# Performance work log

Measured on AMD Instinct MI355X. Metric: run time of the kernel, lower is better.

The kernel has to match this reference:

```python
import jax, jax.numpy as jnp
import numpy as np

P = np.pi
PARENTS = np.array([0,0,0,0,1,2,3,4,5,6,7,8,9,9,9,12,13,14,16,17,18,19,20,21])
VERTS_LIST = np.array([1325,336,1032,4515,1374,4848,1739,5209,1960,5423])
SYNTH = np.array([3,15,4,5,7,8,18,19,20,21])

def _bounds():
    b = [[-0.5933865286111969,0.5933865286111969],[-2*P,2*P],[-1.215762200416361,1.215762200416361],
         [-1.5793940868065197,0.3097956806],[-0.5881754611,0.5689768556],[-0.5323249722,0.6736965222],
         [-1.5793940868065197,0.3097956806],[-0.5689768556,0.5881754611],[-0.6736965222,0.5323249722],
         [-P/3,P/3],[-P/36,P/36],[-P/36,P/36],
         [-0.02268926111,2.441713561],[-0.01,0.01],[-0.01,0.01],
         [-0.02268926111,2.441713561],[-0.01,0.01],[-0.01,0.01],
         [-P/3,P/3],[-P/36,P/36],[-P/36,P/36]]
    b += [[-P/6,P/6]]*6
    b += [[-P/3,P/3],[-P/36,P/36],[-P/36,P/36]]
    b += [[-0.01,0.01]]*6
    b += [[-P/3,P/3],[-P/36,P/36],[-P/36,P/36]]
    k = [(-1.551596394,2.206094311),(-2.455676183,0.7627082389),(-1.570795,2.188641033),
         (-1.551596394,2.206094311),(-0.7627082389,2.455676183),(-2.188641033,1.570795)]
    b += [[a/3.0,c/3.0] for a,c in k]
    b += [[-P/3,P/3],[-P/36,P/36],[-P/36,P/36]]
    b += [[a*2.0/3.0,c*2.0/3.0] for a,c in k]
    b += [[-0.01,0.01],[-2.570867817,0.04799651389],[-0.01,0.01],[-0.01,0.01],[-0.04799651389,2.570867817],[-0.01,0.01]]
    b += [[-P/6,P/6]]*6
    b += [[-0.01,0.01]]*6
    return 2.0*jnp.asarray(np.array(b, np.float32))  # [72,2]

def quat2mat(q):
    q = q / jnp.linalg.norm(q, axis=1, keepdims=True)
    w, x, y, z = q[:,0], q[:,1], q[:,2], q[:,3]
    r0 = jnp.stack([1-2*(y*y+z*z), 2*(x*y-w*z), 2*(x*z+w*y)], -1)
    r1 = jnp.stack([2*(x*y+w*z), 1-2*(x*x+z*z), 2*(y*z-w*x)], -1)
    r2 = jnp.stack([2*(x*z-w*y), 2*(y*z+w*x), 1-2*(x*x+y*y)], -1)
    return jnp.stack([r0, r1, r2], 1)

def batch_rodrigues(theta):  # [N,3] axis-angle -> [N,3,3]
    angle = jnp.linalg.norm(theta + 1e-8, axis=1, keepdims=True)
    half = angle * 0.5
    q = jnp.concatenate([jnp.cos(half), (theta/angle)*jnp.sin(half)], axis=1)
    return quat2mat(q)

def global_rigid_transform(Rs, Js):  # Rs [B,24,3,3], Js [B,24,3]
    B = Rs.shape[0]
    dt = Rs.dtype
    def make_A(R, t):
        Rh = jnp.concatenate([R, jnp.zeros((B,1,3), dt)], axis=1)       # [B,4,3]
        th = jnp.concatenate([t, jnp.ones((B,1), dt)], axis=1)[:,:,None] # [B,4,1]
        return jnp.concatenate([Rh, th], axis=2)                          # [B,4,4]
    results = [make_A(Rs[:,0], Js[:,0])]
    for i in range(1, 24):  # fixed 24-joint kinematic chain
        p = int(PARENTS[i])
        results.append(results[p] @ make_A(Rs[:,i], Js[:,i]-Js[:,p]))
    G = jnp.stack(results, axis=1)  # [B,24,4,4]
    new_J = G[:,:,:3,3]
    Jh = jnp.concatenate([Js, jnp.zeros((B,24,1), dt)], axis=2)[...,None]
    init_bone = jnp.pad(G @ Jh, ((0,0),(0,0),(0,0),(3,0)))
    return new_J, G - init_bone

def setup_inputs():
    key = jax.random.key(0)
    ks = jax.random.split(key, 7)
    B, R = 256, 6890
    x = jax.random.normal(ks[0], (B, 88), jnp.float32)
    g = jax.nn.one_hot(jax.random.randint(ks[1], (B,), 0, 2), 2, dtype=jnp.float32)
    v_template = jax.random.normal(ks[2], (2, R, 3), jnp.float32) * 0.3
    shapedirs = jax.random.normal(ks[3], (2, 10, R, 3), jnp.float32) * 0.01
    Jr = jax.random.uniform(ks[4], (2, R, 24), jnp.float32) ** 8
    J_regressor = Jr / Jr.sum(axis=1, keepdims=True)
    posedirs = jax.random.normal(ks[5], (2, R, 3, 207), jnp.float32) * 0.01
    w = jax.random.uniform(ks[6], (2, R, 24), jnp.float32) ** 8
    weights = w / w.sum(axis=2, keepdims=True)
    return {"x": x, "batch_gender": g, "v_template": v_template, "shapedirs": shapedirs,
            "J_regressor": J_regressor, "posedirs": posedirs, "weights": weights}

def reference(x, batch_gender, v_template, shapedirs, J_regressor, posedirs, weights):
    B = x.shape[0]
    bounds = _bounds()
    # is_gt=False path: root-shift offsets, then pad 88->91 with the atan2 root angles spliced in
    x = x.at[:,10].add(0.6-0.286).at[:,11].add(1.2-0.286).at[:,12].add(0.1)
    betas = jnp.tanh(x[:, :10] / 3.0) * 3.0
    root_shift = x[:, 10:13]
    root_angles = x[:, 13:19]
    root_rot = jnp.stack([jnp.arctan2(x[:,16], x[:,13]),
                          jnp.arctan2(x[:,17], x[:,14]),
                          jnp.arctan2(x[:,18], x[:,15])], axis=1)
    pose = jnp.concatenate([root_rot, x[:, 19:88]], axis=1)  # [B,72]
    mean_b = bounds.mean(axis=1)
    scale = 2.0 / jnp.abs(bounds[:,0] - bounds[:,1])
    pose = jnp.tanh((pose - mean_b) * scale) / scale + mean_b
    Rs = batch_rodrigues(pose.reshape(-1, 3)).reshape(B, 24, 3, 3)
    g = batch_gender  # [B,2]
    vt = jnp.einsum('bg,grd->brd', g, v_template)
    bsm = jnp.einsum('bk,gkrd->gbrd', betas, shapedirs)  # per-gender shape blendshapes
    v_shaped = jnp.einsum('bg,gbrd->brd', g, bsm) + vt   # [B,R,3]
    Jg = jnp.einsum('brd,grj->bgjd', v_shaped, J_regressor)
    J = jnp.einsum('bg,bgjd->bjd', g, Jg)  # [B,24,3]
    new_J, A = global_rigid_transform(Rs, J)
    new_J = new_J - J[:, 0:1] + root_shift[:, None, :]
    pose_feat = (Rs[:, 1:] - jnp.eye(3, dtype=Rs.dtype)).reshape(B, 207)
    pcon = jnp.einsum('bp,grdp->gbrd', pose_feat, posedirs)  # per-gender pose blendshapes
    v_posed = jnp.einsum('bg,gbrd->brd', g, pcon) + v_shaped
    w = jnp.einsum('bg,grj->brj', g, weights)             # [B,R,24]
    T = jnp.einsum('brj,bjpq->brpq', w, A)                # [B,R,4,4]
    verts = jnp.einsum('brij,brj->bri', T[:,:,:3,:3], v_posed) + T[:,:,:3,3]
    verts = verts - J[:, 0:1] + root_shift[:, None, :]
    verts_red = verts[:, VERTS_LIST, :]
    verts_offset = jax.lax.stop_gradient(verts_red) - jax.lax.stop_gradient(new_J[:, SYNTH, :])
    return betas, pose, root_shift, root_angles, verts, verts_red, new_J, verts_offset
```

## Files before the change

### kernel.cpp

```cpp
#include <hip/hip_runtime.h>
#include <hip/hip_bf16.h>


#define NB 256
#define NR 6890
#define NJ 24
#define RD3 (NR*3)
#define KPD 207
#define K2C 8
#define K2R 862
#define NT4 431
#define BROW 232
#define VROW 133

#define OFF_BETAS 0
#define OFF_POSE  2560
#define OFF_RSH   20992
#define OFF_RA    21760
#define OFF_VERTS 23296
#define OFF_VRED  5314816
#define OFF_NEWJ  5322496
#define OFF_VOFF  5340928

#define WS_RS    0
#define WS_PF    55296
#define WS_BETA  108288
#define WS_RSH   110848
#define WS_GI    111616
#define WS_ORD   111872
#define WS_CNT   112128
#define WS_PFB   112904
#define WS_AT    170248

typedef short v8s __attribute__((ext_vector_type(8)));
typedef float v4f __attribute__((ext_vector_type(4)));

__constant__ int PAR_c[24] = {0,0,0,0,1,2,3,4,5,6,7,8,9,9,9,12,13,14,16,17,18,19,20,21};
__constant__ int VL_c[10]  = {1325,336,1032,4515,1374,4848,1739,5209,1960,5423};
__constant__ int SY_c[10]  = {3,15,4,5,7,8,18,19,20,21};
__constant__ int LVL_j[23]  = {1,2,3, 4,5,6, 7,8,9, 10,11,12,13,14, 15,16,17, 18,19, 20,21, 22,23};
__constant__ int LVL_off[9] = {0,3,6,9,14,17,19,21,23};

__constant__ float BLO[72] = {
  -0.5933865286111969f, -6.283185307179586f, -1.215762200416361f,
  -1.5793940868065197f, -0.5881754611f, -0.5323249722f,
  -1.5793940868065197f, -0.5689768556f, -0.6736965222f,
  -1.0471975511965976f, -0.08726646259971647f, -0.08726646259971647f,
  -0.02268926111f, -0.01f, -0.01f,
  -0.02268926111f, -0.01f, -0.01f,
  -1.0471975511965976f, -0.08726646259971647f, -0.08726646259971647f,
  -0.5235987755982988f, -0.5235987755982988f, -0.5235987755982988f,
  -0.5235987755982988f, -0.5235987755982988f, -0.5235987755982988f,
  -1.0471975511965976f, -0.08726646259971647f, -0.08726646259971647f,
  -0.01f, -0.01f, -0.01f, -0.01f, -0.01f, -0.01f,
  -1.0471975511965976f, -0.08726646259971647f, -0.08726646259971647f,
  (float)(-1.551596394/3.0), (float)(-2.455676183/3.0), (float)(-1.570795/3.0),
  (float)(-1.551596394/3.0), (float)(-0.7627082389/3.0), (float)(-2.188641033/3.0),
  -1.0471975511965976f, -0.08726646259971647f, -0.08726646259971647f,
  (float)(-1.551596394*2.0/3.0), (float)(-2.455676183*2.0/3.0), (float)(-1.570795*2.0/3.0),
  (float)(-1.551596394*2.0/3.0), (float)(-0.7627082389*2.0/3.0), (float)(-2.188641033*2.0/3.0),
  -0.01f, -2.570867817f, -0.01f, -0.01f, -0.04799651389f, -0.01f,
  -0.5235987755982988f, -0.5235987755982988f, -0.5235987755982988f,
  -0.5235987755982988f, -0.5235987755982988f, -0.5235987755982988f,
  -0.01f, -0.01f, -0.01f, -0.01f, -0.01f, -0.01f
};
__constant__ float BHI[72] = {
  0.5933865286111969f, 6.283185307179586f, 1.215762200416361f,
  0.3097956806f, 0.5689768556f, 0.6736965222f,
  0.3097956806f, 0.5881754611f, 0.5323249722f,
  1.0471975511965976f, 0.08726646259971647f, 0.08726646259971647f,
  2.441713561f, 0.01f, 0.01f,
  2.441713561f, 0.01f, 0.01f,
  1.0471975511965976f, 0.08726646259971647f, 0.08726646259971647f,
  0.5235987755982988f, 0.5235987755982988f, 0.5235987755982988f,
  0.5235987755982988f, 0.5235987755982988f, 0.5235987755982988f,
  1.0471975511965976f, 0.08726646259971647f, 0.08726646259971647f,
  0.01f, 0.01f, 0.01f, 0.01f, 0.01f, 0.01f,
  1.0471975511965976f, 0.08726646259971647f, 0.08726646259971647f,
  (float)(2.206094311/3.0), (float)(0.7627082389/3.0), (float)(2.188641033/3.0),
  (float)(2.206094311/3.0), (float)(2.455676183/3.0), (float)(1.570795/3.0),
  1.0471975511965976f, 0.08726646259971647f, 0.08726646259971647f,
  (float)(2.206094311*2.0/3.0), (float)(0.7627082389*2.0/3.0), (float)(2.188641033*2.0/3.0),
  (float)(2.206094311*2.0/3.0), (float)(2.455676183*2.0/3.0), (float)(1.570795*2.0/3.0),
  0.01f, 0.04799651389f, 0.01f, 0.01f, 2.570867817f, 0.01f,
  0.5235987755982988f, 0.5235987755982988f, 0.5235987755982988f,
  0.5235987755982988f, 0.5235987755982988f, 0.5235987755982988f,
  0.01f, 0.01f, 0.01f, 0.01f, 0.01f, 0.01f
};

__device__ __forceinline__ unsigned short f2bf(float f) {
  union { float f; unsigned u; } c; c.f = f;
  const unsigned u = c.u + 0x7FFFu + ((c.u >> 16) & 1u);
  return (unsigned short)(u >> 16);
}
__device__ __forceinline__ float bf2f(unsigned short h) {
  union { unsigned u; float f; } c; c.u = (unsigned)h << 16; return c.f;
}

__global__ void kA_front(const float* __restrict__ x, const float* __restrict__ gen,
                         const float* __restrict__ vtemp, const float* __restrict__ sdirs,
                         const float* __restrict__ jreg,
                         float* __restrict__ out, float* __restrict__ W)
{
  const int bid = blockIdx.x;
  const int tid = threadIdx.x;

  if (bid < NB) {
    const int b = bid;
    const float* xb = x + b * 88;
    if (tid < 24) {
      const int j = tid;
      float t[3];
      if (j == 0) {
        t[0] = atan2f(xb[16], xb[13]);
        t[1] = atan2f(xb[17], xb[14]);
        t[2] = atan2f(xb[18], xb[15]);
      } else {
        t[0] = xb[19 + (j - 1) * 3 + 0];
        t[1] = xb[19 + (j - 1) * 3 + 1];
        t[2] = xb[19 + (j - 1) * 3 + 2];
      }
#pragma unroll
      for (int c = 0; c < 3; c++) {
        const int pi = j * 3 + c;
        const float lo = 2.f * BLO[pi], hi = 2.f * BHI[pi];
        const float mean = 0.5f * (lo + hi);
        const float scale = 2.f / fabsf(lo - hi);
        const float v = tanhf((t[c] - mean) * scale) / scale + mean;
        t[c] = v;
        out[OFF_POSE + b * 72 + pi] = v;
      }
      const float a0 = t[0] + 1e-8f, a1 = t[1] + 1e-8f, a2 = t[2] + 1e-8f;
      const float ang = sqrtf(a0 * a0 + a1 * a1 + a2 * a2);
      const float half = 0.5f * ang;
      const float sh = sinf(half), ch = cosf(half);
      const float inv = sh / ang;
      float qw = ch, qx = t[0] * inv, qy = t[1] * inv, qz = t[2] * inv;
      const float nn = sqrtf(qw * qw + qx * qx + qy * qy + qz * qz);
      qw /= nn; qx /= nn; qy /= nn; qz /= nn;
      float R[9];
      R[0] = 1.f - 2.f * (qy * qy + qz * qz); R[1] = 2.f * (qx * qy - qw * qz); R[2] = 2.f * (qx * qz + qw * qy);
      R[3] = 2.f * (qx * qy + qw * qz); R[4] = 1.f - 2.f * (qx * qx + qz * qz); R[5] = 2.f * (qy * qz - qw * qx);
      R[6] = 2.f * (qx * qz - qw * qy); R[7] = 2.f * (qy * qz + qw * qx); R[8] = 1.f - 2.f * (qx * qx + qy * qy);
      float* rsw = W + WS_RS + (size_t)(b * 24 + j) * 9;
#pragma unroll
      for (int e = 0; e < 9; e++) rsw[e] = R[e];
      if (j >= 1) {
        float* pfw = W + WS_PF + (size_t)b * 207 + (j - 1) * 9;
#pragma unroll
        for (int e = 0; e < 9; e++)
          pfw[e] = R[e] - ((e == 0 || e == 4 || e == 8) ? 1.f : 0.f);
      }
    } else if (tid < 34) {
      const int k = tid - 24;
      const float v = tanhf(xb[k] / 3.0f) * 3.0f;
      out[OFF_BETAS + b * 10 + k] = v;
      W[WS_BETA + b * 10 + k] = v;
    } else if (tid == 34) {
      const float r0 = xb[10] + (0.6f - 0.286f);
      const float r1 = xb[11] + (1.2f - 0.286f);
      const float r2 = xb[12] + 0.1f;
      out[OFF_RSH + b * 3 + 0] = r0; out[OFF_RSH + b * 3 + 1] = r1; out[OFF_RSH + b * 3 + 2] = r2;
      W[WS_RSH + b * 3 + 0] = r0; W[WS_RSH + b * 3 + 1] = r1; W[WS_RSH + b * 3 + 2] = r2;
#pragma unroll
      for (int k2 = 0; k2 < 6; k2++) out[OFF_RA + b * 6 + k2] = xb[13 + k2];
    } else if (tid == 35) {
      ((int*)(W + WS_GI))[b] = (gen[b * 2 + 1] > gen[b * 2 + 0]) ? 1 : 0;
    }
    return;
  }

  const int kb = bid - NB;
  const int c = kb % K2C, j = (kb / K2C) % 24, g = kb / (K2C * 24);
  const int r0 = c * K2R;
  int r1 = r0 + K2R; if (r1 > NR) r1 = NR;
  const float* vtg = vtemp + (size_t)g * NR * 3;
  const float* sdg = sdirs + (size_t)g * 10 * NR * 3;
  const float* jrg = jreg + (size_t)g * NR * 24;
  float acc[33];
#pragma unroll
  for (int e = 0; e < 33; e++) acc[e] = 0.f;
  for (int r = r0 + tid; r < r1; r += 256) {
    const float w = jrg[r * 24 + j];
    acc[0] += vtg[r * 3 + 0] * w;
    acc[1] += vtg[r * 3 + 1] * w;
    acc[2] += vtg[r * 3 + 2] * w;
#pragma unroll
    for (int k = 0; k < 10; k++) {
      const float* s = sdg + ((size_t)k * NR + r) * 3;
      acc[3 + k * 3 + 0] += s[0] * w;
      acc[3 + k * 3 + 1] += s[1] * w;
      acc[3 + k * 3 + 2] += s[2] * w;
    }
  }
  __shared__ float red[4][33];
  const int lane = tid & 63, wv = tid >> 6;
#pragma unroll
  for (int e = 0; e < 33; e++) {
    float v = acc[e];
    v += __shfl_down(v, 32); v += __shfl_down(v, 16); v += __shfl_down(v, 8);
    v += __shfl_down(v, 4);  v += __shfl_down(v, 2);  v += __shfl_down(v, 1);
    if (lane == 0) red[wv][e] = v;
  }
  __syncthreads();
  if (tid < 33) {
    const int e = tid;
    out[OFF_VERTS + (size_t)(((g * 24 + j) * K2C + c) * 33 + e)] =
        red[0][e] + red[1][e] + red[2][e] + red[3][e];
  }
}

__global__ void kB_mid(float* __restrict__ out, float* __restrict__ W)
{
  const int bid = blockIdx.x;
  const int tid = threadIdx.x;

  if (bid < 512) {
    __shared__ int s_ord[NB];
    __shared__ int s_c0[4];
    const int gib = ((const int*)(W + WS_GI))[tid];
    const int lane = tid & 63, wvi = tid >> 6;
    const unsigned long long b0 = __ballot(gib == 0);
    if (lane == 0) s_c0[wvi] = __popcll(b0);
    __syncthreads();
    const int t0 = s_c0[0] + s_c0[1] + s_c0[2] + s_c0[3];
    int off0 = 0, off1 = t0;
    for (int w = 0; w < wvi; w++) { off0 += s_c0[w]; off1 += 64 - s_c0[w]; }
    const unsigned long long ltm = (1ull << lane) - 1ull;
    const int rr0 = __popcll(b0 & ltm);
    const int rr1 = lane - rr0;
    if (gib == 0) s_ord[off0 + rr0] = tid;
    else          s_ord[off1 + rr1] = tid;
    __syncthreads();

    if (bid == 0) {
      ((int*)(W + WS_ORD))[tid] = s_ord[tid];
      if (tid == 0) { ((int*)(W + WS_CNT))[0] = t0; ((int*)(W + WS_CNT))[1] = NB - t0; }
    }

    const int g = bid >> 8, m = bid & 255;
    const int n_g = g ? (NB - t0) : t0;
    const int g0off = g ? t0 : 0;
    if (tid < 224) {
      float v = 0.f;
      if (m < n_g) {
        const int b = s_ord[g0off + m];
        if (tid < KPD)        v = W[WS_PF + (size_t)b * KPD + tid];
        else if (tid < 217)   v = W[WS_BETA + b * 10 + (tid - KPD)];
        else if (tid == 217)  v = 1.f;
      }
      ((unsigned short*)(W + WS_PFB))[((size_t)g * 256 + m) * 224 + tid] = f2bf(v);
    }
    return;
  }

  const int b = bid - 512;
  __shared__ float J[72];
  __shared__ float G[24][12];
  __shared__ float sA[24][12];
  __shared__ float j0s[3];
  const int gi = ((const int*)(W + WS_GI))[b];
  float bb[10];
#pragma unroll
  for (int k = 0; k < 10; k++) bb[k] = W[WS_BETA + b * 10 + k];

  if (tid < 72) {
    const int j = tid / 3, d = tid % 3;
    float v = 0.f;
#pragma unroll
    for (int c = 0; c < K2C; c++) {
      const float* P = out + OFF_VERTS + (size_t)(((gi * 24 + j) * K2C + c) * 33);
      float s = P[d];
#pragma unroll
      for (int k = 0; k < 10; k++) s += bb[k] * P[3 + k * 3 + d];
      v += s;
    }
    J[tid] = v;
  }
  __syncthreads();
  const float* Rs = W + WS_RS + (size_t)b * 216;
  if (tid < 12) {
    const int row = tid / 4, col = tid % 4;
    G[0][tid] = (col < 3) ? Rs[row * 3 + col] : J[row];
  }
  __syncthreads();
#pragma unroll
  for (int L = 0; L < 8; L++) {
    const int base = LVL_off[L];
    const int cntL = LVL_off[L + 1] - base;
    const int slot = tid / 12, e = tid - slot * 12;
    if (slot < cntL) {
      const int i = LVL_j[base + slot];
      const int p = PAR_c[i];
      const int row = e / 4, col = e - row * 4;
      const float* Ri = Rs + i * 9;
      const float g0 = G[p][row * 4 + 0], g1 = G[p][row * 4 + 1], g2 = G[p][row * 4 + 2];
      float v;
      if (col < 3) {
        v = g0 * Ri[col] + g1 * Ri[3 + col] + g2 * Ri[6 + col];
      } else {
        const float t0 = J[i * 3 + 0] - J[p * 3 + 0];
        const float t1 = J[i * 3 + 1] - J[p * 3 + 1];
        const float t2 = J[i * 3 + 2] - J[p * 3 + 2];
        v = g0 * t0 + g1 * t1 + g2 * t2 + G[p][row * 4 + 3];
      }
      G[i][e] = v;
    }
    __syncthreads();
  }
  if (tid < 3)
    j0s[tid] = W[WS_RSH + b * 3 + tid] - J[tid];
  __syncthreads();
  if (tid < 72) {
    const int j = tid / 3, d = tid % 3;
    out[OFF_NEWJ + (size_t)b * 72 + tid] = G[j][d * 4 + 3] + j0s[d];
  }
  for (int e = tid; e < 288; e += 256) {
    const int j = e / 12, rc = e - j * 12, row = rc / 4, col = rc - row * 4;
    float v = G[j][rc];
    if (col == 3)
      v -= G[j][row * 4 + 0] * J[j * 3 + 0] + G[j][row * 4 + 1] * J[j * 3 + 1] + G[j][row * 4 + 2] * J[j * 3 + 2];
    sA[j][rc] = v;
  }
  __syncthreads();
  unsigned short* at = (unsigned short*)(W + WS_AT) + (size_t)b * 768;
  for (int e = tid; e < 384; e += 256) {
    const int c = e >> 5, j = e & 31;
    float a = 0.f;
    if (j < 24) a = sA[j][c];
    else if (j == 24) a = ((c & 3) == 3) ? j0s[c >> 2] : 0.f;
    const unsigned short h = f2bf(a);
    const unsigned short l = f2bf(a - bf2f(h));
    at[c * 32 + j] = h;
    at[384 + c * 32 + j] = l;
  }
}

__launch_bounds__(512, 6)
__global__ void k4_fused(const float* __restrict__ pd, const float* __restrict__ vtemp,
                         const float* __restrict__ sdirs, const float* __restrict__ wts,
                         float* __restrict__ out, const float* __restrict__ W)
{
  __shared__ __align__(16) unsigned short bsm[48][BROW];
  __shared__ float vps[48][VROW];
  __shared__ int s_ord[NB];

  const int tid = threadIdx.x;
  const int wave = tid >> 6, lane = tid & 63;
  const int g = blockIdx.y >> 1, h = blockIdx.y & 1;
  const int nfrac = lane & 15;
  const int kq = (lane >> 4) * 8;
  const int tile = blockIdx.x;
  const int n0 = tile * 48;
  const int rbase = tile * 16;

  const int* cnt = (const int*)(W + WS_CNT);
  const int* ord = (const int*)(W + WS_ORD);
  const int n_g = cnt[g];
  const int g0off = g ? cnt[0] : 0;
  int nh = n_g - h * 128; if (nh > 128) nh = 128;
  if (nh <= 0) return;

  if (tid < NB) s_ord[tid] = ord[tid];

  const int nrows = (RD3 - n0 < 48) ? (RD3 - n0) : 48;
  const int nflat = nrows * KPD;
  const float* src = pd + ((size_t)g * RD3 + n0) * KPD;
#pragma unroll
  for (int i = 0; i < 5; i++) {
    const int e4 = (i * 512 + tid) * 4;
    if (e4 + 3 < nflat) {
      float v[4];
      __builtin_memcpy(v, src + e4, 16);
#pragma unroll
      for (int t = 0; t < 4; t++) {
        const int fl = e4 + t;
        bsm[fl / KPD][fl % KPD] = f2bf(v[t]);
      }
    } else if (e4 < nflat) {
      for (int t = 0; t < 4 && e4 + t < nflat; t++)
        bsm[(e4 + t) / KPD][(e4 + t) % KPD] = f2bf(src[e4 + t]);
    }
  }
  if (tid < 48) {
    const int nr = (n0 + tid < RD3) ? (n0 + tid) : (RD3 - 1);
    const int rr = nr / 3, dd = nr - rr * 3;
#pragma unroll
    for (int kk = 0; kk < 10; kk++)
      bsm[tid][KPD + kk] = f2bf(sdirs[((size_t)(g * 10 + kk) * NR + rr) * 3 + dd]);
    bsm[tid][217] = f2bf(vtemp[((size_t)g * NR + rr) * 3 + dd]);
#pragma unroll
    for (int kk = 218; kk < 224; kk++) bsm[tid][kk] = 0;
  }
  __syncthreads();

  const unsigned short* pfb = (const unsigned short*)(W + WS_PFB) + (size_t)g * 256 * 224;
  const int mtmax_h = (nh + 15) >> 4;
  const int ntasks = 3 * mtmax_h;
  for (int t = wave; t < ntasks; t += 8) {
    const int s = t % 3, mt = t / 3;
    const unsigned short* bp = &bsm[s * 16 + nfrac][0];
    v8s bfr[7];
#pragma unroll
    for (int c = 0; c < 7; c++) bfr[c] = *(const v8s*)(bp + c * 32 + kq);
    const unsigned short* ap = pfb + (size_t)(h * 128 + mt * 16 + nfrac) * 224 + kq;
    v8s af[7];
#pragma unroll
    for (int c = 0; c < 7; c++) af[c] = *(const v8s*)(ap + c * 32);

    v4f acc0 = {0.f, 0.f, 0.f, 0.f};
    v4f acc1 = {0.f, 0.f, 0.f, 0.f};
    acc0 = __builtin_amdgcn_mfma_f32_16x16x32_bf16(af[0], bfr[0], acc0, 0, 0, 0);
    acc1 = __builtin_amdgcn_mfma_f32_16x16x32_bf16(af[1], bfr[1], acc1, 0, 0, 0);
    acc0 = __builtin_amdgcn_mfma_f32_16x16x32_bf16(af[2], bfr[2], acc0, 0, 0, 0);
    acc1 = __builtin_amdgcn_mfma_f32_16x16x32_bf16(af[3], bfr[3], acc1, 0, 0, 0);
    acc0 = __builtin_amdgcn_mfma_f32_16x16x32_bf16(af[4], bfr[4], acc0, 0, 0, 0);
    acc1 = __builtin_amdgcn_mfma_f32_16x16x32_bf16(af[5], bfr[5], acc1, 0, 0, 0);
    acc0 = __builtin_amdgcn_mfma_f32_16x16x32_bf16(af[6], bfr[6], acc0, 0, 0, 0);

    const int ln = s * 16 + nfrac;
    const int lm0 = mt * 16 + (lane >> 4) * 4;
#pragma unroll
    for (int j = 0; j < 4; j++)
      vps[ln][lm0 + j] = acc0[j] + acc1[j];
  }
  __syncthreads();

  const int f = nfrac, q = lane >> 4;
  const int r = rbase + f;
  const int rc = (r < NR) ? r : (NR - 1);

  int vli = -1;
#pragma unroll
  for (int i = 0; i < 10; i++) if (r == VL_c[i]) vli = i;
  const int syj = (vli >= 0) ? SY_c[vli] : 0;

  v8s wh, wl;
  {
    union { v8s v; unsigned short s[8]; } H, L;
    if (q < 3) {
      float fw[8];
      __builtin_memcpy(fw, wts + ((size_t)g * NR + rc) * 24 + q * 8, 32);
#pragma unroll
      for (int t = 0; t < 8; t++) { H.s[t] = f2bf(fw[t]); L.s[t] = f2bf(fw[t] - bf2f(H.s[t])); }
    } else {
#pragma unroll
      for (int t = 0; t < 8; t++) { H.s[t] = (t == 0) ? 0x3F80 : 0; L.s[t] = 0; }
    }
    wh = H.v; wl = L.v;
  }

  const unsigned short* at = (const unsigned short*)(W + WS_AT);
  const int fragoff = f * 32 + q * 8;

  for (int lm = wave; lm < nh; lm += 8) {
    const int b = s_ord[g0off + h * 128 + lm];
    const v8s ah = *(const v8s*)(at + (size_t)b * 768 + fragoff);
    const v8s al = *(const v8s*)(at + (size_t)b * 768 + 384 + fragoff);
    const float vx = vps[f * 3 + 0][lm];
    const float vy = vps[f * 3 + 1][lm];
    const float vz = vps[f * 3 + 2][lm];

    v4f acc = {0.f, 0.f, 0.f, 0.f};
    acc = __builtin_amdgcn_mfma_f32_16x16x32_bf16(ah, wh, acc, 0, 0, 0);
    acc = __builtin_amdgcn_mfma_f32_16x16x32_bf16(ah, wl, acc, 0, 0, 0);
    acc = __builtin_amdgcn_mfma_f32_16x16x32_bf16(al, wh, acc, 0, 0, 0);
    const float o = acc[0] * vx + acc[1] * vy + acc[2] * vz + acc[3];
    if (q < 3 && r < NR) {
      out[OFF_VERTS + ((size_t)b * NR + r) * 3 + q] = o;
      if (vli >= 0) {
        out[OFF_VRED + ((size_t)b * 10 + vli) * 3 + q] = o;
        out[OFF_VOFF + ((size_t)b * 10 + vli) * 3 + q] =
            o - out[OFF_NEWJ + (size_t)b * 72 + syj * 3 + q];
      }
    }
  }
}

extern "C" void kernel_launch(void* const* d_in, const int* in_sizes, int n_in,
                              void* d_out, int out_size, void* d_ws, size_t ws_size,
                              hipStream_t stream)
{
  const float* x   = (const float*)d_in[0];
  const float* gen = (const float*)d_in[1];
  const float* vt  = (const float*)d_in[2];
  const float* sd  = (const float*)d_in[3];
  const float* jr  = (const float*)d_in[4];
  const float* pd  = (const float*)d_in[5];
  const float* wt  = (const float*)d_in[6];
  float* out = (float*)d_out;
  float* W   = (float*)d_ws;

  kA_front<<<NB + 2 * 24 * K2C, 256, 0, stream>>>(x, gen, vt, sd, jr, out, W);
  kB_mid<<<512 + NB, 256, 0, stream>>>(out, W);
  k4_fused<<<dim3(NT4, 4), 512, 0, stream>>>(pd, vt, sd, wt, out, W);
}
```

Before: 76.04 us.

## Merge batch halves per block, store blend results as bf16, unroll skinning loop

Each block now covers all batch rows for one gender instead of splitting them into two halves. This halves the grid and stops the posedirs tile from being loaded and converted twice. The intermediate vps buffer is stored in bf16 to cut shared memory, and the skinning loop processes two batch rows per iteration with interleaved MFMAs. Posedir loads are issued all at once before conversion, and the extra-column setup is spread across more threads. The risks are lower per-block parallelism, bf16 rounding of the posed vertex values, and higher register pressure.

```diff
diff --git a/kernel.cpp b/kernel.cpp
--- a/kernel.cpp
+++ b/kernel.cpp
@@ -11,7 +11,7 @@
 #define K2R 862
 #define NT4 431
 #define BROW 232
-#define VROW 133
+#define VROWB 264
 
 #define OFF_BETAS 0
 #define OFF_POSE  2560
@@ -342,12 +342,12 @@
                          float* __restrict__ out, const float* __restrict__ W)
 {
   __shared__ __align__(16) unsigned short bsm[48][BROW];
-  __shared__ float vps[48][VROW];
+  __shared__ __align__(16) unsigned short vps[48][VROWB];
   __shared__ int s_ord[NB];
 
   const int tid = threadIdx.x;
   const int wave = tid >> 6, lane = tid & 63;
-  const int g = blockIdx.y >> 1, h = blockIdx.y & 1;
+  const int g = blockIdx.y;
   const int nfrac = lane & 15;
   const int kq = (lane >> 4) * 8;
   const int tile = blockIdx.x;
@@ -356,9 +356,8 @@
 
   const int* cnt = (const int*)(W + WS_CNT);
   const int* ord = (const int*)(W + WS_ORD);
-  const int n_g = cnt[g];
+  const int nh = cnt[g];
   const int g0off = g ? cnt[0] : 0;
-  int nh = n_g - h * 128; if (nh > 128) nh = 128;
   if (nh <= 0) return;
 
   if (tid < NB) s_ord[tid] = ord[tid];
@@ -366,63 +365,79 @@
   const int nrows = (RD3 - n0 < 48) ? (RD3 - n0) : 48;
   const int nflat = nrows * KPD;
   const float* src = pd + ((size_t)g * RD3 + n0) * KPD;
-#pragma unroll
-  for (int i = 0; i < 5; i++) {
-    const int e4 = (i * 512 + tid) * 4;
-    if (e4 + 3 < nflat) {
-      float v[4];
-      __builtin_memcpy(v, src + e4, 16);
+  {
+    float v[20];
+#pragma unroll
+    for (int i = 0; i < 5; i++) {
+      const int e4 = (i * 512 + tid) * 4;
+      if (e4 + 3 < nflat) {
+        float t4[4];
+        __builtin_memcpy(t4, src + e4, 16);
+        v[i * 4 + 0] = t4[0]; v[i * 4 + 1] = t4[1]; v[i * 4 + 2] = t4[2]; v[i * 4 + 3] = t4[3];
+      } else {
+#pragma unroll
+        for (int t = 0; t < 4; t++)
+          v[i * 4 + t] = (e4 + t < nflat) ? src[e4 + t] : 0.f;
+      }
+    }
+#pragma unroll
+    for (int i = 0; i < 5; i++) {
+      const int e4 = (i * 512 + tid) * 4;
 #pragma unroll
       for (int t = 0; t < 4; t++) {
         const int fl = e4 + t;
-        bsm[fl / KPD][fl % KPD] = f2bf(v[t]);
-      }
-    } else if (e4 < nflat) {
-      for (int t = 0; t < 4 && e4 + t < nflat; t++)
-        bsm[(e4 + t) / KPD][(e4 + t) % KPD] = f2bf(src[e4 + t]);
-    }
-  }
-  if (tid < 48) {
-    const int nr = (n0 + tid < RD3) ? (n0 + tid) : (RD3 - 1);
+        if (fl < nflat) bsm[fl / KPD][fl % KPD] = f2bf(v[i * 4 + t]);
+      }
+    }
+  }
+  if (tid < 480) {
+    const int r_ = tid / 10, kk = tid - r_ * 10;
+    const int nr = (n0 + r_ < RD3) ? (n0 + r_) : (RD3 - 1);
     const int rr = nr / 3, dd = nr - rr * 3;
-#pragma unroll
-    for (int kk = 0; kk < 10; kk++)
-      bsm[tid][KPD + kk] = f2bf(sdirs[((size_t)(g * 10 + kk) * NR + rr) * 3 + dd]);
-    bsm[tid][217] = f2bf(vtemp[((size_t)g * NR + rr) * 3 + dd]);
-#pragma unroll
-    for (int kk = 218; kk < 224; kk++) bsm[tid][kk] = 0;
+    bsm[r_][KPD + kk] = f2bf(sdirs[((size_t)(g * 10 + kk) * NR + rr) * 3 + dd]);
+  }
+  if (tid >= 464) {
+    const int r_ = tid - 464;
+    const int nr = (n0 + r_ < RD3) ? (n0 + r_) : (RD3 - 1);
+    const int rr = nr / 3, dd = nr - rr * 3;
+    bsm[r_][217] = f2bf(vtemp[((size_t)g * NR + rr) * 3 + dd]);
+  }
+  if (tid < 288) {
+    const int r_ = tid / 6, kk = 218 + (tid - r_ * 6);
+    bsm[r_][kk] = 0;
   }
   __syncthreads();
 
   const unsigned short* pfb = (const unsigned short*)(W + WS_PFB) + (size_t)g * 256 * 224;
-  const int mtmax_h = (nh + 15) >> 4;
-  const int ntasks = 3 * mtmax_h;
-  for (int t = wave; t < ntasks; t += 8) {
-    const int s = t % 3, mt = t / 3;
+  const int mtmax = (nh + 15) >> 4;
+#pragma unroll
+  for (int s = 0; s < 3; s++) {
     const unsigned short* bp = &bsm[s * 16 + nfrac][0];
     v8s bfr[7];
 #pragma unroll
     for (int c = 0; c < 7; c++) bfr[c] = *(const v8s*)(bp + c * 32 + kq);
-    const unsigned short* ap = pfb + (size_t)(h * 128 + mt * 16 + nfrac) * 224 + kq;
-    v8s af[7];
-#pragma unroll
-    for (int c = 0; c < 7; c++) af[c] = *(const v8s*)(ap + c * 32);
-
-    v4f acc0 = {0.f, 0.f, 0.f, 0.f};
-    v4f acc1 = {0.f, 0.f, 0.f, 0.f};
-    acc0 = __builtin_amdgcn_mfma_f32_16x16x32_bf16(af[0], bfr[0], acc0, 0, 0, 0);
-    acc1 = __builtin_amdgcn_mfma_f32_16x16x32_bf16(af[1], bfr[1], acc1, 0, 0, 0);
-    acc0 = __builtin_amdgcn_mfma_f32_16x16x32_bf16(af[2], bfr[2], acc0, 0, 0, 0);
-    acc1 = __builtin_amdgcn_mfma_f32_16x16x32_bf16(af[3], bfr[3], acc1, 0, 0, 0);
-    acc0 = __builtin_amdgcn_mfma_f32_16x16x32_bf16(af[4], bfr[4], acc0, 0, 0, 0);
-    acc1 = __builtin_amdgcn_mfma_f32_16x16x32_bf16(af[5], bfr[5], acc1, 0, 0, 0);
-    acc0 = __builtin_amdgcn_mfma_f32_16x16x32_bf16(af[6], bfr[6], acc0, 0, 0, 0);
-
-    const int ln = s * 16 + nfrac;
-    const int lm0 = mt * 16 + (lane >> 4) * 4;
-#pragma unroll
-    for (int j = 0; j < 4; j++)
-      vps[ln][lm0 + j] = acc0[j] + acc1[j];
+    for (int mt = wave; mt < mtmax; mt += 8) {
+      const unsigned short* ap = pfb + (size_t)(mt * 16 + nfrac) * 224 + kq;
+      v8s af[7];
+#pragma unroll
+      for (int c = 0; c < 7; c++) af[c] = *(const v8s*)(ap + c * 32);
+
+      v4f acc0 = {0.f, 0.f, 0.f, 0.f};
+      v4f acc1 = {0.f, 0.f, 0.f, 0.f};
+      acc0 = __builtin_amdgcn_mfma_f32_16x16x32_bf16(af[0], bfr[0], acc0, 0, 0, 0);
+      acc1 = __builtin_amdgcn_mfma_f32_16x16x32_bf16(af[1], bfr[1], acc1, 0, 0, 0);
+      acc0 = __builtin_amdgcn_mfma_f32_16x16x32_bf16(af[2], bfr[2], acc0, 0, 0, 0);
+      acc1 = __builtin_amdgcn_mfma_f32_16x16x32_bf16(af[3], bfr[3], acc1, 0, 0, 0);
+      acc0 = __builtin_amdgcn_mfma_f32_16x16x32_bf16(af[4], bfr[4], acc0, 0, 0, 0);
+      acc1 = __builtin_amdgcn_mfma_f32_16x16x32_bf16(af[5], bfr[5], acc1, 0, 0, 0);
+      acc0 = __builtin_amdgcn_mfma_f32_16x16x32_bf16(af[6], bfr[6], acc0, 0, 0, 0);
+
+      const int ln = s * 16 + nfrac;
+      const int lm0 = mt * 16 + (lane >> 4) * 4;
+#pragma unroll
+      for (int j = 0; j < 4; j++)
+        vps[ln][lm0 + j] = f2bf(acc0[j] + acc1[j]);
+    }
   }
   __syncthreads();
 
@@ -453,25 +468,46 @@
   const unsigned short* at = (const unsigned short*)(W + WS_AT);
   const int fragoff = f * 32 + q * 8;
 
-  for (int lm = wave; lm < nh; lm += 8) {
-    const int b = s_ord[g0off + h * 128 + lm];
-    const v8s ah = *(const v8s*)(at + (size_t)b * 768 + fragoff);
-    const v8s al = *(const v8s*)(at + (size_t)b * 768 + 384 + fragoff);
-    const float vx = vps[f * 3 + 0][lm];
-    const float vy = vps[f * 3 + 1][lm];
-    const float vz = vps[f * 3 + 2][lm];
-
-    v4f acc = {0.f, 0.f, 0.f, 0.f};
-    acc = __builtin_amdgcn_mfma_f32_16x16x32_bf16(ah, wh, acc, 0, 0, 0);
-    acc = __builtin_amdgcn_mfma_f32_16x16x32_bf16(ah, wl, acc, 0, 0, 0);
-    acc = __builtin_amdgcn_mfma_f32_16x16x32_bf16(al, wh, acc, 0, 0, 0);
-    const float o = acc[0] * vx + acc[1] * vy + acc[2] * vz + acc[3];
+  for (int lm = wave; lm < nh; lm += 16) {
+    const int lmB = lm + 8;
+    const bool hasB = (lmB < nh);
+    const int lmBc = hasB ? lmB : lm;
+    const int b1 = s_ord[g0off + lm];
+    const int b2 = s_ord[g0off + lmBc];
+    const v8s ah1 = *(const v8s*)(at + (size_t)b1 * 768 + fragoff);
+    const v8s al1 = *(const v8s*)(at + (size_t)b1 * 768 + 384 + fragoff);
+    const v8s ah2 = *(const v8s*)(at + (size_t)b2 * 768 + fragoff);
+    const v8s al2 = *(const v8s*)(at + (size_t)b2 * 768 + 384 + fragoff);
+    const float vx1 = bf2f(vps[f * 3 + 0][lm]);
+    const float vy1 = bf2f(vps[f * 3 + 1][lm]);
+    const float vz1 = bf2f(vps[f * 3 + 2][lm]);
+    const float vx2 = bf2f(vps[f * 3 + 0][lmBc]);
+    const float vy2 = bf2f(vps[f * 3 + 1][lmBc]);
+    const float vz2 = bf2f(vps[f * 3 + 2][lmBc]);
+
+    v4f accA = {0.f, 0.f, 0.f, 0.f};
+    v4f accB = {0.f, 0.f, 0.f, 0.f};
+    accA = __builtin_amdgcn_mfma_f32_16x16x32_bf16(ah1, wh, accA, 0, 0, 0);
+    accB = __builtin_amdgcn_mfma_f32_16x16x32_bf16(ah2, wh, accB, 0, 0, 0);
+    accA = __builtin_amdgcn_mfma_f32_16x16x32_bf16(ah1, wl, accA, 0, 0, 0);
+    accB = __builtin_amdgcn_mfma_f32_16x16x32_bf16(ah2, wl, accB, 0, 0, 0);
+    accA = __builtin_amdgcn_mfma_f32_16x16x32_bf16(al1, wh, accA, 0, 0, 0);
+    accB = __builtin_amdgcn_mfma_f32_16x16x32_bf16(al2, wh, accB, 0, 0, 0);
+
+    const float o1 = accA[0] * vx1 + accA[1] * vy1 + accA[2] * vz1 + accA[3];
+    const float o2 = accB[0] * vx2 + accB[1] * vy2 + accB[2] * vz2 + accB[3];
     if (q < 3 && r < NR) {
-      out[OFF_VERTS + ((size_t)b * NR + r) * 3 + q] = o;
+      out[OFF_VERTS + ((size_t)b1 * NR + r) * 3 + q] = o1;
+      if (hasB) out[OFF_VERTS + ((size_t)b2 * NR + r) * 3 + q] = o2;
       if (vli >= 0) {
-        out[OFF_VRED + ((size_t)b * 10 + vli) * 3 + q] = o;
-        out[OFF_VOFF + ((size_t)b * 10 + vli) * 3 + q] =
-            o - out[OFF_NEWJ + (size_t)b * 72 + syj * 3 + q];
+        out[OFF_VRED + ((size_t)b1 * 10 + vli) * 3 + q] = o1;
+        out[OFF_VOFF + ((size_t)b1 * 10 + vli) * 3 + q] =
+            o1 - out[OFF_NEWJ + (size_t)b1 * 72 + syj * 3 + q];
+        if (hasB) {
+          out[OFF_VRED + ((size_t)b2 * 10 + vli) * 3 + q] = o2;
+          out[OFF_VOFF + ((size_t)b2 * 10 + vli) * 3 + q] =
+              o2 - out[OFF_NEWJ + (size_t)b2 * 72 + syj * 3 + q];
+        }
       }
     }
   }
@@ -493,5 +529,5 @@
 
   kA_front<<<NB + 2 * 24 * K2C, 256, 0, stream>>>(x, gen, vt, sd, jr, out, W);
   kB_mid<<<512 + NB, 256, 0, stream>>>(out, W);
-  k4_fused<<<dim3(NT4, 4), 512, 0, stream>>>(pd, vt, sd, wt, out, W);
+  k4_fused<<<dim3(NT4, 2), 512, 0, stream>>>(pd, vt, sd, wt, out, W);
 }
```

Measured after the change: 77.93 us. +2.5%, slower.
